# Optimization experiments

Measured on AMD Instinct MI355X. Metric: run time of the kernel, lower is better.

## Reference

```python
import jax, jax.numpy as jnp
import numpy as np

SIM_THRESHOLD = 0.6  # similarity_threshold from __init__
H, W = 96, 96
N = H * W
T = 64


def setup_inputs() -> dict:
    key = jax.random.key(0)
    spike_trace = jax.random.uniform(key, (1, T, N), dtype=jnp.float32)
    return {
        "spike_trace": spike_trace,
        "classifier_start_step": 32,
        "image_height": H,
        "image_width": W,
    }


def reference(spike_trace, classifier_start_step, image_height, image_width):
    B, num_steps, num_pixels = spike_trace.shape
    start_idx = min(max(classifier_start_step - 1, 0), num_steps - 1)
    # average late spikes -> per-pixel scalar value
    pixel_values = spike_trace[:, start_idx:, :].mean(axis=1)[0]  # [N]
    # pairwise similarity: 1 - |v_i - v_j|  -> [N, N]
    similarity = 1.0 - jnp.abs(pixel_values[:, None] - pixel_values[None, :])
    adj = similarity >= SIM_THRESHOLD  # [N, N] bool, diagonal always True

    # Connected components via min-label propagation (data-parallel
    # equivalent of the original sequential DFS).
    init_labels = jnp.arange(num_pixels, dtype=jnp.int32)
    sentinel = jnp.int32(num_pixels)

    def cond(state):
        return state[1]

    def body(state):
        labels, _ = state
        neigh_min = jnp.min(jnp.where(adj, labels[None, :], sentinel), axis=1)
        new_labels = jnp.minimum(neigh_min, labels)
        return new_labels, jnp.any(new_labels != labels)

    labels, _ = jax.lax.while_loop(cond, body, (init_labels, jnp.bool_(True)))

    # masks[c] = indicator of the component whose minimum pixel index is c.
    # Rows c that are not a component root are all-zero (fixed-shape padded
    # form of the torch output; compacting nonzero rows in ascending c order
    # reproduces torch.stack(component_masks) exactly, since DFS start pixels
    # are exactly the component minimum indices, visited in ascending order).
    masks = (labels[None, :] == init_labels[:, None]).astype(spike_trace.dtype)
    masks = masks.reshape(num_pixels, image_height, image_width)
    mean_spike_grid = pixel_values.reshape(image_height, image_width)
    return masks, mean_spike_grid
```

## Files before the change

kernel.cpp:

```cpp
#include <hip/hip_runtime.h>


#define N_PIX 9216

__global__ void k_means(const float* __restrict__ spike, const int* __restrict__ cs_p,
                        int T, float* __restrict__ v, float* __restrict__ out_grid,
                        int* __restrict__ compmin, int* __restrict__ ngaps) {
    int n = blockIdx.x * blockDim.x + threadIdx.x;
    if (n >= N_PIX) return;
    int cs = cs_p[0];
    int start = cs - 1;
    if (start < 0) start = 0;
    if (start > T - 1) start = T - 1;
    float s = 0.0f;
    for (int t = start; t < T; ++t)
        s += spike[(size_t)t * N_PIX + n];
    float val = s / (float)(T - start);
    v[n] = val;
    out_grid[n] = val;
    compmin[n] = 0x7fffffff;
    if (n == 0) *ngaps = 0;
}

__global__ void __launch_bounds__(256) k_gaps(const float* __restrict__ v,
                                              float* __restrict__ gaps,
                                              int* __restrict__ ngaps) {
    int k = blockIdx.x;
    float vk = v[k];
    int hasG = 0, hasAdj = 0;
    for (int j = threadIdx.x; j < N_PIX; j += 256) {
        float vj = v[j];
        if (vj > vk) {
            hasG = 1;
            if (1.0f - (vj - vk) >= 0.6f) hasAdj = 1;
        }
    }
    __shared__ int sG, sA;
    if (threadIdx.x == 0) { sG = 0; sA = 0; }
    __syncthreads();
    if (hasG)   atomicOr(&sG, 1);
    if (hasAdj) atomicOr(&sA, 1);
    __syncthreads();
    if (threadIdx.x == 0 && sG && !sA) {
        int idx = atomicAdd(ngaps, 1);
        gaps[idx] = vk;
    }
}

__global__ void k_ids(const float* __restrict__ v, const float* __restrict__ gaps,
                      const int* __restrict__ ngaps, int* __restrict__ gid,
                      int* __restrict__ compmin) {
    int i = blockIdx.x * blockDim.x + threadIdx.x;
    if (i >= N_PIX) return;
    float vi = v[i];
    int ng = *ngaps;
    int g = 0;
    for (int t = 0; t < ng; ++t) g += (gaps[t] < vi) ? 1 : 0;
    gid[i] = g;
    atomicMin(&compmin[g], i);
}

__global__ void k_scatter(const int* __restrict__ gid, const int* __restrict__ compmin,
                          float* __restrict__ out) {
    int n = blockIdx.x * blockDim.x + threadIdx.x;
    if (n >= N_PIX) return;
    int label = compmin[gid[n]];
    out[(size_t)label * N_PIX + n] = 1.0f;
}

extern "C" void kernel_launch(void* const* d_in, const int* in_sizes, int n_in,
                              void* d_out, int out_size, void* d_ws, size_t ws_size,
                              hipStream_t stream) {
    const float* spike = (const float*)d_in[0];
    const int* cs = (const int*)d_in[1];
    int T = in_sizes[0] / N_PIX;

    float* out = (float*)d_out;
    float* out_grid = out + (size_t)N_PIX * N_PIX;

    float* v       = (float*)d_ws;
    float* gaps    = v + N_PIX;
    int*   ngaps   = (int*)(gaps + N_PIX);
    int*   gid     = ngaps + 4;
    int*   compmin = gid + N_PIX;

    hipMemsetAsync(out, 0, (size_t)N_PIX * N_PIX * sizeof(float), stream);

    k_means  <<<(N_PIX + 255) / 256, 256, 0, stream>>>(spike, cs, T, v, out_grid, compmin, ngaps);
    k_gaps   <<<N_PIX, 256, 0, stream>>>(v, gaps, ngaps);
    k_ids    <<<(N_PIX + 255) / 256, 256, 0, stream>>>(v, gaps, ngaps, gid, compmin);
    k_scatter<<<(N_PIX + 255) / 256, 256, 0, stream>>>(gid, compmin, out);
}
```

Baseline: 488.9 us.

## Replace memset plus scatter with single row-wise mask writer using nontemporal stores

Drops the hipMemsetAsync of the large mask output and the scattered writes of ones. A new labels kernel records each pixel's root and flags root rows, and a per-row writer kernel writes each output row once with vectorized nontemporal stores, all zeros for non-root rows and comparison results for root rows. This removes one full pass over the output and the separate scatter kernel, at the cost of an extra kernel launch and a labels read for each root row.

```diff
diff --git a/kernel.cpp b/kernel.cpp
--- a/kernel.cpp
+++ b/kernel.cpp
@@ -3,9 +3,13 @@
 
 #define N_PIX 9216
 
+typedef float  f32x4 __attribute__((ext_vector_type(4)));
+typedef int    i32x4 __attribute__((ext_vector_type(4)));
+
 __global__ void k_means(const float* __restrict__ spike, const int* __restrict__ cs_p,
                         int T, float* __restrict__ v, float* __restrict__ out_grid,
-                        int* __restrict__ compmin, int* __restrict__ ngaps) {
+                        int* __restrict__ compmin, int* __restrict__ is_root,
+                        int* __restrict__ ngaps) {
     int n = blockIdx.x * blockDim.x + threadIdx.x;
     if (n >= N_PIX) return;
     int cs = cs_p[0];
@@ -19,6 +23,7 @@
     v[n] = val;
     out_grid[n] = val;
     compmin[n] = 0x7fffffff;
+    is_root[n] = 0;
     if (n == 0) *ngaps = 0;
 }
 
@@ -60,12 +65,41 @@
     atomicMin(&compmin[g], i);
 }
 
-__global__ void k_scatter(const int* __restrict__ gid, const int* __restrict__ compmin,
-                          float* __restrict__ out) {
+__global__ void k_labels(const int* __restrict__ gid, const int* __restrict__ compmin,
+                         int* __restrict__ labels, int* __restrict__ is_root) {
     int n = blockIdx.x * blockDim.x + threadIdx.x;
     if (n >= N_PIX) return;
-    int label = compmin[gid[n]];
-    out[(size_t)label * N_PIX + n] = 1.0f;
+    int lab = compmin[gid[n]];
+    labels[n] = lab;
+    is_root[lab] = 1;
+}
+
+__global__ void __launch_bounds__(256) k_write(const int* __restrict__ labels,
+                                               const int* __restrict__ is_root,
+                                               float* __restrict__ out) {
+    int r = blockIdx.x;
+    f32x4* orow = reinterpret_cast<f32x4*>(out + (size_t)r * N_PIX);
+    if (is_root[r] == 0) {
+        const f32x4 z = {0.f, 0.f, 0.f, 0.f};
+        #pragma unroll
+        for (int it = 0; it < (N_PIX / 4) / 256; ++it) {
+            int i = it * 256 + threadIdx.x;
+            __builtin_nontemporal_store(z, &orow[i]);
+        }
+    } else {
+        const i32x4* lab4 = reinterpret_cast<const i32x4*>(labels);
+        #pragma unroll
+        for (int it = 0; it < (N_PIX / 4) / 256; ++it) {
+            int i = it * 256 + threadIdx.x;
+            i32x4 l = lab4[i];
+            f32x4 m;
+            m.x = (l.x == r) ? 1.0f : 0.0f;
+            m.y = (l.y == r) ? 1.0f : 0.0f;
+            m.z = (l.z == r) ? 1.0f : 0.0f;
+            m.w = (l.w == r) ? 1.0f : 0.0f;
+            __builtin_nontemporal_store(m, &orow[i]);
+        }
+    }
 }
 
 extern "C" void kernel_launch(void* const* d_in, const int* in_sizes, int n_in,
@@ -83,11 +117,13 @@
     int*   ngaps   = (int*)(gaps + N_PIX);
     int*   gid     = ngaps + 4;
     int*   compmin = gid + N_PIX;
+    int*   labels  = compmin + N_PIX;
+    int*   is_root = labels + N_PIX;
 
-    hipMemsetAsync(out, 0, (size_t)N_PIX * N_PIX * sizeof(float), stream);
-
-    k_means  <<<(N_PIX + 255) / 256, 256, 0, stream>>>(spike, cs, T, v, out_grid, compmin, ngaps);
+    k_means  <<<(N_PIX + 255) / 256, 256, 0, stream>>>(spike, cs, T, v, out_grid,
+                                                       compmin, is_root, ngaps);
     k_gaps   <<<N_PIX, 256, 0, stream>>>(v, gaps, ngaps);
     k_ids    <<<(N_PIX + 255) / 256, 256, 0, stream>>>(v, gaps, ngaps, gid, compmin);
-    k_scatter<<<(N_PIX + 255) / 256, 256, 0, stream>>>(gid, compmin, out);
+    k_labels <<<(N_PIX + 255) / 256, 256, 0, stream>>>(gid, compmin, labels, is_root);
+    k_write  <<<N_PIX, 256, 0, stream>>>(labels, is_root, out);
 }
```

Measured after the change: 500.0 us. 2.3% more time.
